# Kernel optimization log

Measured on AMD Instinct MI355X. Metric: run time of the kernel, lower is better.

Reference implementation:

```python
import jax, jax.numpy as jnp
import numpy as np

B, D_IN, H, D_OUT = 1024, 512, 512, 512


def _act(v):
    # torch.relu(x) ** 2
    r = jnp.maximum(v, 0.0)
    return r * r


def setup_inputs() -> dict:
    key = jax.random.key(0)
    ks = jax.random.split(key, 8)
    x = jax.random.normal(ks[0], (B, D_IN), dtype=jnp.float32)
    # input_to_hidden: Linear(D_IN, H)
    W_in = jax.random.normal(ks[1], (D_IN, H), dtype=jnp.float32) / np.sqrt(D_IN)
    b_in = jax.random.normal(ks[2], (H,), dtype=jnp.float32) * 0.01
    # hidden_to_hidden[i]: Linear(1, H-i-1). Pack into padded arrays [H-1, H]
    # where row i, column j is the weight feeding output index j (valid only j > i).
    W_hh = jax.random.normal(ks[3], (H - 1, H), dtype=jnp.float32) * 0.02
    b_hh = jax.random.normal(ks[4], (H - 1, H), dtype=jnp.float32) * 0.01
    # hidden_to_output: Linear(H, D_OUT)
    W_out = jax.random.normal(ks[5], (H, D_OUT), dtype=jnp.float32) / np.sqrt(H)
    b_out = jax.random.normal(ks[6], (D_OUT,), dtype=jnp.float32) * 0.01
    return {"x": x, "W_in": W_in, "b_in": b_in, "W_hh": W_hh, "b_hh": b_hh,
            "W_out": W_out, "b_out": b_out}


def reference(x, W_in, b_in, W_hh, b_hh, W_out, b_out):
    h0 = _act(x @ W_in + b_in)  # [B, H]
    hid = h0.shape[1]
    col = jnp.arange(hid)

    def step(h, inp):
        i, w, b = inp  # w, b: [H] padded rows
        src = jnp.take(h, i, axis=1)  # [B], uses UPDATED h (strict sequential dep)
        contrib = _act(src[:, None] * w[None, :] + b[None, :])  # [B, H]
        mask = (col > i).astype(h.dtype)  # only columns i+1.. get updated
        return h + contrib * mask[None, :], None

    xs = (jnp.arange(hid - 1), W_hh, b_hh)
    h, _ = jax.lax.scan(step, h0, xs)
    return h @ W_out + b_out  # [B, D_OUT]
```

## Files before the change

kernel.cpp:

```cpp
#include <hip/hip_runtime.h>

#define B_SZ 1024
#define DIN 512
#define HH 512
#define DOUT 512

typedef short bf16x8 __attribute__((ext_vector_type(8)));
typedef float f32x4 __attribute__((ext_vector_type(4)));

__device__ __forceinline__ unsigned short f2bf(float f) {
    unsigned int u = __float_as_uint(f);
    u += 0x7FFFu + ((u >> 16) & 1u);
    return (unsigned short)(u >> 16);
}
__device__ __forceinline__ float bf2f(unsigned short s) {
    return __uint_as_float(((unsigned int)s) << 16);
}

__device__ __forceinline__ uint4 cvt8(const float4& a0, const float4& a1, int term) {
    const float av[8] = {a0.x, a0.y, a0.z, a0.w, a1.x, a1.y, a1.z, a1.w};
    unsigned int p[4];
    #pragma unroll
    for (int q = 0; q < 4; ++q) {
        float f0 = av[2 * q], f1 = av[2 * q + 1];
        unsigned short h0 = f2bf(f0), h1 = f2bf(f1);
        if (term == 1) { h0 = f2bf(f0 - bf2f(h0)); h1 = f2bf(f1 - bf2f(h1)); }
        p[q] = (unsigned int)h0 | ((unsigned int)h1 << 16);
    }
    uint4 v; v.x = p[0]; v.y = p[1]; v.z = p[2]; v.w = p[3];
    return v;
}

__device__ __forceinline__ void convW_body(const float* __restrict__ W,
                                           uint4* __restrict__ dst, int t) {
    const int lane = t & 63;
    const int fb   = t >> 6;
    const int ks   = fb >> 5;
    const int nf   = fb & 31;
    const int col  = nf * 16 + (lane & 15);
    const int kb   = ks * 32 + ((lane >> 4) << 3);
    const int term = kb >> 9;
    const int c0   = kb & 511;
    unsigned short o[8];
    #pragma unroll
    for (int j = 0; j < 8; ++j) {
        const float f = W[(size_t)(c0 + j) * 512 + col];
        unsigned short hi = f2bf(f);
        o[j] = (term == 2) ? f2bf(f - bf2f(hi)) : hi;
    }
    uint4 v;
    v.x = (unsigned int)o[0] | ((unsigned int)o[1] << 16);
    v.y = (unsigned int)o[2] | ((unsigned int)o[3] << 16);
    v.z = (unsigned int)o[4] | ((unsigned int)o[5] << 16);
    v.w = (unsigned int)o[6] | ((unsigned int)o[7] << 16);
    dst[t] = v;
}

template <int C>
__device__ __forceinline__ void pack_bulk(const float* __restrict__ W_hh,
                                          const float* __restrict__ b_hh,
                                          float2* __restrict__ wbk, int e) {
    constexpr int NK = 7 - C;
    constexpr int CB = (C==0?0:C==1?7:C==2?13:C==3?18:C==4?22:C==5?25:27) * 4096;
    const int s   = e / (NK * 64);
    const int rem = e - s * (NK * 64);
    const int row = 64 * C + s;
    const int col = 64 * (C + 1) + rem;
    float2 o;
    o.x = W_hh[(size_t)row * 512 + col];
    o.y = b_hh[(size_t)row * 512 + col];
    wbk[CB + e] = o;
}

__global__ __launch_bounds__(256)
void prep_all(const float* __restrict__ W_hh, const float* __restrict__ b_hh,
              float2* __restrict__ wdg, float2* __restrict__ wbk,
              const float* __restrict__ W_in, uint4* __restrict__ Bin,
              const float* __restrict__ W_out, uint4* __restrict__ Bout) {
    const int b = blockIdx.x;
    const int tid = threadIdx.x;
    if (b < 128) {
        const int idx = b * 256 + tid;
        const int i = idx >> 6, l = idx & 63;
        float2 o;
        if (i < 511 && l > (i & 63)) {
            const int col = ((i >> 6) << 6) + l;
            o.x = W_hh[(size_t)i * 512 + col];
            o.y = b_hh[(size_t)i * 512 + col];
        } else { o.x = 0.0f; o.y = -1.0f; }
        wdg[idx] = o;
    } else if (b < 576) {
        const int rb = b - 128;
        if      (rb < 112) pack_bulk<0>(W_hh, b_hh, wbk, (rb      ) * 256 + tid);
        else if (rb < 208) pack_bulk<1>(W_hh, b_hh, wbk, (rb - 112) * 256 + tid);
        else if (rb < 288) pack_bulk<2>(W_hh, b_hh, wbk, (rb - 208) * 256 + tid);
        else if (rb < 352) pack_bulk<3>(W_hh, b_hh, wbk, (rb - 288) * 256 + tid);
        else if (rb < 400) pack_bulk<4>(W_hh, b_hh, wbk, (rb - 352) * 256 + tid);
        else if (rb < 432) pack_bulk<5>(W_hh, b_hh, wbk, (rb - 400) * 256 + tid);
        else               pack_bulk<6>(W_hh, b_hh, wbk, (rb - 432) * 256 + tid);
    } else if (b < 960) {
        convW_body(W_in, Bin, (b - 576) * 256 + tid);
    } else {
        convW_body(W_out, Bout, (b - 960) * 256 + tid);
    }
}

template <bool ACT>
__global__ __launch_bounds__(512, 2)
void mfma_gemm(const float* __restrict__ A,
               const uint4* __restrict__ Bg,
               const float* __restrict__ bias,
               float* __restrict__ C) {
    __shared__ uint4 lds[2][768];
    const int tid  = threadIdx.x;
    const int lane = tid & 63;
    const int w    = tid >> 6;
    const int mfw  = w & 3;
    const int nfw  = w >> 2;
    const int mf0  = blockIdx.x * 4;
    const int nf0  = blockIdx.y * 2;

    const int ks_s = tid >> 8;
    const int mf_s = (tid >> 6) & 3;
    const int arow = (mf0 + mf_s) * 16 + (lane & 15);
    const int koff = (lane >> 4) << 3;
    const int bks  = tid >> 7;
    const int bnf  = (tid >> 6) & 1;

    float4 Ra0, Ra1; uint4 R2;
    auto stage = [&](int s) {
        const int kp = (s * 2 + ks_s) * 32 + koff;
        const int c  = kp & 511;
        Ra0 = *(const float4*)&A[(size_t)arow * 512 + c];
        Ra1 = *(const float4*)&A[(size_t)arow * 512 + c + 4];
        if (tid < 256)
            R2 = Bg[(size_t)((s * 2 + bks) * 32 + nf0 + bnf) * 64 + lane];
    };
    auto write_tile = [&](int buf, int s) {
        const int kp = (s * 2 + ks_s) * 32 + koff;
        lds[buf][ks_s * 256 + mf_s * 64 + lane] = cvt8(Ra0, Ra1, kp >> 9);
        if (tid < 256)
            lds[buf][512 + bks * 128 + bnf * 64 + lane] = R2;
    };

    f32x4 acc = {0.f, 0.f, 0.f, 0.f};

    stage(0);
    write_tile(0, 0);
    stage(1);
    __syncthreads();

    for (int s = 0; s < 24; ++s) {
        const int cur = s & 1;
        if (s + 1 < 24) write_tile(cur ^ 1, s + 1);
        if (s + 2 < 24) stage(s + 2);
        __builtin_amdgcn_sched_barrier(0);

        bf16x8 aF0 = *(const bf16x8*)&lds[cur][        mfw * 64 + lane];
        bf16x8 aF1 = *(const bf16x8*)&lds[cur][256   + mfw * 64 + lane];
        bf16x8 bF0 = *(const bf16x8*)&lds[cur][512   + nfw * 64 + lane];
        bf16x8 bF1 = *(const bf16x8*)&lds[cur][512+128 + nfw * 64 + lane];
        acc = __builtin_amdgcn_mfma_f32_16x16x32_bf16(aF0, bF0, acc, 0, 0, 0);
        acc = __builtin_amdgcn_mfma_f32_16x16x32_bf16(aF1, bF1, acc, 0, 0, 0);
        __syncthreads();
    }

    const int colg  = (nf0 + nfw) * 16 + (lane & 15);
    const float bv  = bias[colg];
    const int rbase = (mf0 + mfw) * 16 + ((lane >> 4) << 2);
    #pragma unroll
    for (int r = 0; r < 4; ++r) {
        float v = acc[r] + bv;
        if (ACT) { v = fmaxf(v, 0.f); v = v * v; }
        C[(size_t)(rbase + r) * 512 + colg] = v;
    }
}

template <int C>
__device__ __forceinline__ void scan_chunk(const float2* __restrict__ wdg,
                                           const float2* __restrict__ wbk,
                                           float hr[8], int lane) {
    constexpr int NK = 7 - C;
    constexpr int DD = 16;
    constexpr int D  = (NK >= 6) ? 4 : (NK >= 3) ? 8 : 16;
    constexpr int CB = (C==0?0:C==1?7:C==2?13:C==3?18:C==4?22:C==5?25:C==6?27:28) * 4096;

    const float2* dptr = wdg + (64 * C) * 64 + lane;
    const float2* bptr = wbk + CB + lane;

    __syncthreads();

    float2 Wd[DD];
    #pragma unroll
    for (int q = 0; q < DD; ++q) Wd[q] = dptr[q * 64];

    float2 Wb[NK > 0 ? D : 1][NK > 0 ? NK : 1];
    if constexpr (NK > 0) {
        #pragma unroll
        for (int q = 0; q < D; ++q)
            #pragma unroll
            for (int k = 0; k < NK; ++k)
                Wb[q][k] = bptr[(q * NK + k) * 64];
    }
    __builtin_amdgcn_sched_barrier(0);

    for (int t = 0; t < 64 / DD; ++t) {
        #pragma unroll
        for (int q = 0; q < DD; ++q) {
            const int s = t * DD + q;
            if (!(C == 7 && s == 63)) {
                const float hi = __uint_as_float(
                    __builtin_amdgcn_readlane(__float_as_uint(hr[C]), s));
                const float tv = fmaf(hi, Wd[q].x, Wd[q].y);
                const float rv = fmaxf(tv, 0.f);
                hr[C] = fmaf(rv, rv, hr[C]);
            }
            if (t + 1 < 64 / DD) Wd[q] = dptr[(s + DD) * 64];
        }
        __builtin_amdgcn_s_barrier();
    }

    if constexpr (NK > 0) {
        constexpr int NT = 64 / D;
        for (int t = 0; t < NT; ++t) {
            #pragma unroll
            for (int q = 0; q < D; ++q) {
                const int i = t * D + q;
                const float hi = __uint_as_float(
                    __builtin_amdgcn_readlane(__float_as_uint(hr[C]), i));
                #pragma unroll
                for (int k = 0; k < NK; ++k) {
                    const float tv = fmaf(hi, Wb[q][k].x, Wb[q][k].y);
                    const float rv = fmaxf(tv, 0.f);
                    hr[C + 1 + k] = fmaf(rv, rv, hr[C + 1 + k]);
                }
                if (t + 1 < NT) {
                    const float2* p = bptr + (size_t)(i + D) * (NK * 64);
                    #pragma unroll
                    for (int k = 0; k < NK; ++k)
                        Wb[q][k] = p[k * 64];
                }
            }
            __builtin_amdgcn_s_barrier();
        }
    }
}

__global__ __launch_bounds__(256, 1)
void scan_kernel(const float2* __restrict__ wdg, const float2* __restrict__ wbk,
                 float* __restrict__ h) {
    const int lane = threadIdx.x & 63;
    const int wave = threadIdx.x >> 6;
    const int row  = blockIdx.x * 4 + wave;
    float* hrow = h + (size_t)row * HH;

    float hr[8];
    #pragma unroll
    for (int k = 0; k < 8; ++k) hr[k] = hrow[lane + 64 * k];

    scan_chunk<0>(wdg, wbk, hr, lane);
    scan_chunk<1>(wdg, wbk, hr, lane);
    scan_chunk<2>(wdg, wbk, hr, lane);
    scan_chunk<3>(wdg, wbk, hr, lane);
    scan_chunk<4>(wdg, wbk, hr, lane);
    scan_chunk<5>(wdg, wbk, hr, lane);
    scan_chunk<6>(wdg, wbk, hr, lane);
    scan_chunk<7>(wdg, wbk, hr, lane);

    #pragma unroll
    for (int k = 0; k < 8; ++k) hrow[lane + 64 * k] = hr[k];
}

extern "C" void kernel_launch(void* const* d_in, const int* in_sizes, int n_in,
                              void* d_out, int out_size, void* d_ws, size_t ws_size,
                              hipStream_t stream) {
    const float* x     = (const float*)d_in[0];
    const float* W_in  = (const float*)d_in[1];
    const float* b_in  = (const float*)d_in[2];
    const float* W_hh  = (const float*)d_in[3];
    const float* b_hh  = (const float*)d_in[4];
    const float* W_out = (const float*)d_in[5];
    const float* b_out = (const float*)d_in[6];
    float* out = (float*)d_out;

    char* ws = (char*)d_ws;
    float2* wdg  = (float2*)ws;
    float2* wbk  = (float2*)(ws + 0x040000u);
    float*  h    = (float*)(ws + 0x120000u);
    uint4*  Bin  = (uint4*)(ws + 0x320000u);
    uint4*  Bout = (uint4*)(ws + 0x4A0000u);

    prep_all<<<dim3(1344), dim3(256), 0, stream>>>(W_hh, b_hh, wdg, wbk,
                                                   W_in, Bin, W_out, Bout);

    mfma_gemm<true><<<dim3(16, 16), dim3(512), 0, stream>>>(x, Bin, b_in, h);

    scan_kernel<<<dim3(256), dim3(256), 0, stream>>>(wdg, wbk, h);

    mfma_gemm<false><<<dim3(16, 16), dim3(512), 0, stream>>>(h, Bout, b_out, out);
}
```

Baseline: 175.5 us.

## Stage off-diagonal scan weights through double-buffered LDS shared by block waves

```diff
diff --git a/kernel.cpp b/kernel.cpp
--- a/kernel.cpp
+++ b/kernel.cpp
@@ -179,30 +179,37 @@
 template <int C>
 __device__ __forceinline__ void scan_chunk(const float2* __restrict__ wdg,
                                            const float2* __restrict__ wbk,
-                                           float hr[8], int lane) {
+                                           float2 (* __restrict__ sm)[3584],
+                                           float hr[8], int lane, int tid) {
     constexpr int NK = 7 - C;
     constexpr int DD = 16;
-    constexpr int D  = (NK >= 6) ? 4 : (NK >= 3) ? 8 : 16;
     constexpr int CB = (C==0?0:C==1?7:C==2?13:C==3?18:C==4?22:C==5?25:C==6?27:28) * 4096;
-
-    const float2* dptr = wdg + (64 * C) * 64 + lane;
-    const float2* bptr = wbk + CB + lane;
-
-    __syncthreads();
+    constexpr int TS = (NK >= 4) ? 8 : (NK >= 2) ? 16 : 32;
+    constexpr int NT = 64 / TS;
+    constexpr int IB = (NK > 0) ? (TS * NK / 8) : 1;
+
+    const float2* dptr  = wdg + (64 * C) * 64 + lane;
+    const float4* gbase = (const float4*)(wbk + CB);
+
+    float4 Rst[IB];
+    auto stageR = [&](int t) {
+        const float4* g = gbase + (size_t)t * (TS * NK * 32);
+        #pragma unroll
+        for (int u = 0; u < IB; ++u) Rst[u] = g[u * 256 + tid];
+    };
+    auto writeR = [&](int buf) {
+        float4* l = (float4*)&sm[buf][0];
+        #pragma unroll
+        for (int u = 0; u < IB; ++u) l[u * 256 + tid] = Rst[u];
+    };
+
+    if constexpr (NK > 0) stageR(0);
 
     float2 Wd[DD];
     #pragma unroll
     for (int q = 0; q < DD; ++q) Wd[q] = dptr[q * 64];
 
-    float2 Wb[NK > 0 ? D : 1][NK > 0 ? NK : 1];
-    if constexpr (NK > 0) {
-        #pragma unroll
-        for (int q = 0; q < D; ++q)
-            #pragma unroll
-            for (int k = 0; k < NK; ++k)
-                Wb[q][k] = bptr[(q * NK + k) * 64];
-    }
-    __builtin_amdgcn_sched_barrier(0);
+    if constexpr (NK > 0) { writeR(0); stageR(1); }
 
     for (int t = 0; t < 64 / DD; ++t) {
         #pragma unroll
@@ -217,31 +224,32 @@
             }
             if (t + 1 < 64 / DD) Wd[q] = dptr[(s + DD) * 64];
         }
-        __builtin_amdgcn_s_barrier();
     }
 
     if constexpr (NK > 0) {
-        constexpr int NT = 64 / D;
+        __syncthreads();
         for (int t = 0; t < NT; ++t) {
-            #pragma unroll
-            for (int q = 0; q < D; ++q) {
-                const int i = t * D + q;
+            const int cur = t & 1;
+            if (t + 1 < NT) writeR(cur ^ 1);
+            if (t + 2 < NT) stageR(t + 2);
+            __builtin_amdgcn_sched_barrier(0);
+
+            #pragma unroll 4
+            for (int s = 0; s < TS; ++s) {
                 const float hi = __uint_as_float(
-                    __builtin_amdgcn_readlane(__float_as_uint(hr[C]), i));
+                    __builtin_amdgcn_readlane(__float_as_uint(hr[C]), t * TS + s));
+                float2 wv[NK];
+                #pragma unroll
+                for (int k = 0; k < NK; ++k)
+                    wv[k] = sm[cur][(s * NK + k) * 64 + lane];
                 #pragma unroll
                 for (int k = 0; k < NK; ++k) {
-                    const float tv = fmaf(hi, Wb[q][k].x, Wb[q][k].y);
+                    const float tv = fmaf(hi, wv[k].x, wv[k].y);
                     const float rv = fmaxf(tv, 0.f);
                     hr[C + 1 + k] = fmaf(rv, rv, hr[C + 1 + k]);
                 }
-                if (t + 1 < NT) {
-                    const float2* p = bptr + (size_t)(i + D) * (NK * 64);
-                    #pragma unroll
-                    for (int k = 0; k < NK; ++k)
-                        Wb[q][k] = p[k * 64];
-                }
             }
-            __builtin_amdgcn_s_barrier();
+            __syncthreads();
         }
     }
 }
@@ -249,8 +257,10 @@
 __global__ __launch_bounds__(256, 1)
 void scan_kernel(const float2* __restrict__ wdg, const float2* __restrict__ wbk,
                  float* __restrict__ h) {
-    const int lane = threadIdx.x & 63;
-    const int wave = threadIdx.x >> 6;
+    __shared__ float2 sm[2][3584];
+    const int tid  = threadIdx.x;
+    const int lane = tid & 63;
+    const int wave = tid >> 6;
     const int row  = blockIdx.x * 4 + wave;
     float* hrow = h + (size_t)row * HH;
 
@@ -258,14 +268,14 @@
     #pragma unroll
     for (int k = 0; k < 8; ++k) hr[k] = hrow[lane + 64 * k];
 
-    scan_chunk<0>(wdg, wbk, hr, lane);
-    scan_chunk<1>(wdg, wbk, hr, lane);
-    scan_chunk<2>(wdg, wbk, hr, lane);
-    scan_chunk<3>(wdg, wbk, hr, lane);
-    scan_chunk<4>(wdg, wbk, hr, lane);
-    scan_chunk<5>(wdg, wbk, hr, lane);
-    scan_chunk<6>(wdg, wbk, hr, lane);
-    scan_chunk<7>(wdg, wbk, hr, lane);
+    scan_chunk<0>(wdg, wbk, sm, hr, lane, tid);
+    scan_chunk<1>(wdg, wbk, sm, hr, lane, tid);
+    scan_chunk<2>(wdg, wbk, sm, hr, lane, tid);
+    scan_chunk<3>(wdg, wbk, sm, hr, lane, tid);
+    scan_chunk<4>(wdg, wbk, sm, hr, lane, tid);
+    scan_chunk<5>(wdg, wbk, sm, hr, lane, tid);
+    scan_chunk<6>(wdg, wbk, sm, hr, lane, tid);
+    scan_chunk<7>(wdg, wbk, sm, hr, lane, tid);
 
     #pragma unroll
     for (int k = 0; k < 8; ++k) hrow[lane + 64 * k] = hr[k];
```

Result: slower. 192.4 us (+9.7%).

## Fuse all stages into one cooperative kernel and stage scan weights via LDS

Applied to the files above, without the earlier changes.

```diff
diff --git a/kernel.cpp b/kernel.cpp
--- a/kernel.cpp
+++ b/kernel.cpp
@@ -1,4 +1,7 @@
 #include <hip/hip_runtime.h>
+#include <hip/hip_cooperative_groups.h>
+
+namespace cg = cooperative_groups;
 
 #define B_SZ 1024
 #define DIN 512
@@ -29,6 +32,12 @@
     }
     uint4 v; v.x = p[0]; v.y = p[1]; v.z = p[2]; v.w = p[3];
     return v;
+}
+
+__device__ __forceinline__ void gload_lds16(const void* g, void* l) {
+    __builtin_amdgcn_global_load_lds(
+        (__attribute__((address_space(1))) void*)g,
+        (__attribute__((address_space(3))) void*)l, 16, 0, 0);
 }
 
 __device__ __forceinline__ void convW_body(const float* __restrict__ W,
@@ -72,53 +81,55 @@
     wbk[CB + e] = o;
 }
 
-__global__ __launch_bounds__(256)
-void prep_all(const float* __restrict__ W_hh, const float* __restrict__ b_hh,
-              float2* __restrict__ wdg, float2* __restrict__ wbk,
-              const float* __restrict__ W_in, uint4* __restrict__ Bin,
-              const float* __restrict__ W_out, uint4* __restrict__ Bout) {
-    const int b = blockIdx.x;
-    const int tid = threadIdx.x;
-    if (b < 128) {
-        const int idx = b * 256 + tid;
-        const int i = idx >> 6, l = idx & 63;
-        float2 o;
-        if (i < 511 && l > (i & 63)) {
-            const int col = ((i >> 6) << 6) + l;
-            o.x = W_hh[(size_t)i * 512 + col];
-            o.y = b_hh[(size_t)i * 512 + col];
-        } else { o.x = 0.0f; o.y = -1.0f; }
-        wdg[idx] = o;
-    } else if (b < 576) {
-        const int rb = b - 128;
-        if      (rb < 112) pack_bulk<0>(W_hh, b_hh, wbk, (rb      ) * 256 + tid);
-        else if (rb < 208) pack_bulk<1>(W_hh, b_hh, wbk, (rb - 112) * 256 + tid);
-        else if (rb < 288) pack_bulk<2>(W_hh, b_hh, wbk, (rb - 208) * 256 + tid);
-        else if (rb < 352) pack_bulk<3>(W_hh, b_hh, wbk, (rb - 288) * 256 + tid);
-        else if (rb < 400) pack_bulk<4>(W_hh, b_hh, wbk, (rb - 352) * 256 + tid);
-        else if (rb < 432) pack_bulk<5>(W_hh, b_hh, wbk, (rb - 400) * 256 + tid);
-        else               pack_bulk<6>(W_hh, b_hh, wbk, (rb - 432) * 256 + tid);
-    } else if (b < 960) {
-        convW_body(W_in, Bin, (b - 576) * 256 + tid);
-    } else {
-        convW_body(W_out, Bout, (b - 960) * 256 + tid);
+__device__ __forceinline__ void prep_phase(const float* __restrict__ W_hh,
+                                           const float* __restrict__ b_hh,
+                                           float2* __restrict__ wdg,
+                                           float2* __restrict__ wbk,
+                                           const float* __restrict__ W_in,
+                                           uint4* __restrict__ Bin,
+                                           const float* __restrict__ W_out,
+                                           uint4* __restrict__ Bout,
+                                           int bid, int tid) {
+    for (int gt = bid * 512 + tid; gt < 344064; gt += 131072) {
+        if (gt < 32768) {
+            const int i = gt >> 6, l = gt & 63;
+            float2 o;
+            if (i < 511 && l > (i & 63)) {
+                const int col = ((i >> 6) << 6) + l;
+                o.x = W_hh[(size_t)i * 512 + col];
+                o.y = b_hh[(size_t)i * 512 + col];
+            } else { o.x = 0.0f; o.y = -1.0f; }
+            wdg[gt] = o;
+        } else if (gt < 147456) {
+            const int e = gt - 32768;
+            if      (e < 28672)  pack_bulk<0>(W_hh, b_hh, wbk, e);
+            else if (e < 53248)  pack_bulk<1>(W_hh, b_hh, wbk, e - 28672);
+            else if (e < 73728)  pack_bulk<2>(W_hh, b_hh, wbk, e - 53248);
+            else if (e < 90112)  pack_bulk<3>(W_hh, b_hh, wbk, e - 73728);
+            else if (e < 102400) pack_bulk<4>(W_hh, b_hh, wbk, e - 90112);
+            else if (e < 110592) pack_bulk<5>(W_hh, b_hh, wbk, e - 102400);
+            else                 pack_bulk<6>(W_hh, b_hh, wbk, e - 110592);
+        } else if (gt < 245760) {
+            convW_body(W_in, Bin, gt - 147456);
+        } else {
+            convW_body(W_out, Bout, gt - 245760);
+        }
     }
 }
 
 template <bool ACT>
-__global__ __launch_bounds__(512, 2)
-void mfma_gemm(const float* __restrict__ A,
-               const uint4* __restrict__ Bg,
-               const float* __restrict__ bias,
-               float* __restrict__ C) {
-    __shared__ uint4 lds[2][768];
-    const int tid  = threadIdx.x;
+__device__ __forceinline__ void gemm_body(const float* __restrict__ A,
+                                          const uint4* __restrict__ Bg,
+                                          const float* __restrict__ bias,
+                                          float* __restrict__ Cc,
+                                          uint4 (*lds)[768],
+                                          int bx, int by, int tid) {
     const int lane = tid & 63;
     const int w    = tid >> 6;
     const int mfw  = w & 3;
     const int nfw  = w >> 2;
-    const int mf0  = blockIdx.x * 4;
-    const int nf0  = blockIdx.y * 2;
+    const int mf0  = bx * 4;
+    const int nf0  = by * 2;
 
     const int ks_s = tid >> 8;
     const int mf_s = (tid >> 6) & 3;
@@ -156,9 +167,9 @@
         if (s + 2 < 24) stage(s + 2);
         __builtin_amdgcn_sched_barrier(0);
 
-        bf16x8 aF0 = *(const bf16x8*)&lds[cur][        mfw * 64 + lane];
-        bf16x8 aF1 = *(const bf16x8*)&lds[cur][256   + mfw * 64 + lane];
-        bf16x8 bF0 = *(const bf16x8*)&lds[cur][512   + nfw * 64 + lane];
+        bf16x8 aF0 = *(const bf16x8*)&lds[cur][          mfw * 64 + lane];
+        bf16x8 aF1 = *(const bf16x8*)&lds[cur][256     + mfw * 64 + lane];
+        bf16x8 bF0 = *(const bf16x8*)&lds[cur][512     + nfw * 64 + lane];
         bf16x8 bF1 = *(const bf16x8*)&lds[cur][512+128 + nfw * 64 + lane];
         acc = __builtin_amdgcn_mfma_f32_16x16x32_bf16(aF0, bF0, acc, 0, 0, 0);
         acc = __builtin_amdgcn_mfma_f32_16x16x32_bf16(aF1, bF1, acc, 0, 0, 0);
@@ -172,103 +183,141 @@
     for (int r = 0; r < 4; ++r) {
         float v = acc[r] + bv;
         if (ACT) { v = fmaxf(v, 0.f); v = v * v; }
-        C[(size_t)(rbase + r) * 512 + colg] = v;
+        Cc[(size_t)(rbase + r) * 512 + colg] = v;
     }
 }
 
 template <int C>
 __device__ __forceinline__ void scan_chunk(const float2* __restrict__ wdg,
                                            const float2* __restrict__ wbk,
-                                           float hr[8], int lane) {
+                                           float2* __restrict__ smb,
+                                           float hr[8], int lane, int wave, int tid) {
     constexpr int NK = 7 - C;
-    constexpr int DD = 16;
-    constexpr int D  = (NK >= 6) ? 4 : (NK >= 3) ? 8 : 16;
     constexpr int CB = (C==0?0:C==1?7:C==2?13:C==3?18:C==4?22:C==5?25:C==6?27:28) * 4096;
-
     const float2* dptr = wdg + (64 * C) * 64 + lane;
-    const float2* bptr = wbk + CB + lane;
-
-    __syncthreads();
-
-    float2 Wd[DD];
-    #pragma unroll
-    for (int q = 0; q < DD; ++q) Wd[q] = dptr[q * 64];
-
-    float2 Wb[NK > 0 ? D : 1][NK > 0 ? NK : 1];
+    const char* gchunk = (const char*)(wbk + CB);
+
+    float2 Wd[16];
+    if (wave < 4) {
+        #pragma unroll
+        for (int q = 0; q < 16; ++q) Wd[q] = dptr[q * 64];
+    }
     if constexpr (NK > 0) {
         #pragma unroll
-        for (int q = 0; q < D; ++q)
+        for (int u = 0; u < NK; ++u)
+            gload_lds16(gchunk + (size_t)(u * 512 + tid) * 16,
+                        (char*)smb + (size_t)(u * 512 + wave * 64) * 16);
+    }
+
+    if (wave < 4) {
+        for (int t = 0; t < 4; ++t) {
             #pragma unroll
-            for (int k = 0; k < NK; ++k)
-                Wb[q][k] = bptr[(q * NK + k) * 64];
-    }
-    __builtin_amdgcn_sched_barrier(0);
-
-    for (int t = 0; t < 64 / DD; ++t) {
-        #pragma unroll
-        for (int q = 0; q < DD; ++q) {
-            const int s = t * DD + q;
-            if (!(C == 7 && s == 63)) {
-                const float hi = __uint_as_float(
-                    __builtin_amdgcn_readlane(__float_as_uint(hr[C]), s));
-                const float tv = fmaf(hi, Wd[q].x, Wd[q].y);
-                const float rv = fmaxf(tv, 0.f);
-                hr[C] = fmaf(rv, rv, hr[C]);
+            for (int q = 0; q < 16; ++q) {
+                const int s = t * 16 + q;
+                if (!(C == 7 && s == 63)) {
+                    const float hi = __uint_as_float(
+                        __builtin_amdgcn_readlane(__float_as_uint(hr[C]), s));
+                    const float tv = fmaf(hi, Wd[q].x, Wd[q].y);
+                    const float rv = fmaxf(tv, 0.f);
+                    hr[C] = fmaf(rv, rv, hr[C]);
+                }
+                if (t < 3) Wd[q] = dptr[(s + 16) * 64];
             }
-            if (t + 1 < 64 / DD) Wd[q] = dptr[(s + DD) * 64];
         }
-        __builtin_amdgcn_s_barrier();
     }
 
     if constexpr (NK > 0) {
-        constexpr int NT = 64 / D;
-        for (int t = 0; t < NT; ++t) {
-            #pragma unroll
-            for (int q = 0; q < D; ++q) {
-                const int i = t * D + q;
-                const float hi = __uint_as_float(
-                    __builtin_amdgcn_readlane(__float_as_uint(hr[C]), i));
-                #pragma unroll
-                for (int k = 0; k < NK; ++k) {
-                    const float tv = fmaf(hi, Wb[q][k].x, Wb[q][k].y);
-                    const float rv = fmaxf(tv, 0.f);
-                    hr[C + 1 + k] = fmaf(rv, rv, hr[C + 1 + k]);
-                }
-                if (t + 1 < NT) {
-                    const float2* p = bptr + (size_t)(i + D) * (NK * 64);
+        __syncthreads();
+        for (int t = 0; t < 4; ++t) {
+            if (wave < 4) {
+                #pragma unroll 2
+                for (int s = 0; s < 16; ++s) {
+                    const float hi = __uint_as_float(
+                        __builtin_amdgcn_readlane(__float_as_uint(hr[C]), t * 16 + s));
                     #pragma unroll
-                    for (int k = 0; k < NK; ++k)
-                        Wb[q][k] = p[k * 64];
+                    for (int k = 0; k < NK; ++k) {
+                        const float2 wv = smb[(s * NK + k) * 64 + lane];
+                        const float tv = fmaf(hi, wv.x, wv.y);
+                        const float rv = fmaxf(tv, 0.f);
+                        hr[C + 1 + k] = fmaf(rv, rv, hr[C + 1 + k]);
+                    }
                 }
             }
-            __builtin_amdgcn_s_barrier();
+            __syncthreads();
+            if (t < 3) {
+                #pragma unroll
+                for (int u = 0; u < NK; ++u)
+                    gload_lds16(gchunk + (size_t)((t + 1) * NK * 512 + u * 512 + tid) * 16,
+                                (char*)smb + (size_t)(u * 512 + wave * 64) * 16);
+                __syncthreads();
+            }
         }
     }
 }
 
-__global__ __launch_bounds__(256, 1)
-void scan_kernel(const float2* __restrict__ wdg, const float2* __restrict__ wbk,
-                 float* __restrict__ h) {
-    const int lane = threadIdx.x & 63;
-    const int wave = threadIdx.x >> 6;
-    const int row  = blockIdx.x * 4 + wave;
-    float* hrow = h + (size_t)row * HH;
-
-    float hr[8];
-    #pragma unroll
-    for (int k = 0; k < 8; ++k) hr[k] = hrow[lane + 64 * k];
-
-    scan_chunk<0>(wdg, wbk, hr, lane);
-    scan_chunk<1>(wdg, wbk, hr, lane);
-    scan_chunk<2>(wdg, wbk, hr, lane);
-    scan_chunk<3>(wdg, wbk, hr, lane);
-    scan_chunk<4>(wdg, wbk, hr, lane);
-    scan_chunk<5>(wdg, wbk, hr, lane);
-    scan_chunk<6>(wdg, wbk, hr, lane);
-    scan_chunk<7>(wdg, wbk, hr, lane);
-
-    #pragma unroll
-    for (int k = 0; k < 8; ++k) hrow[lane + 64 * k] = hr[k];
+__device__ __forceinline__ void scan_phase(const float2* __restrict__ wdg,
+                                           const float2* __restrict__ wbk,
+                                           float* __restrict__ h,
+                                           float2* __restrict__ smb,
+                                           int bid, int tid) {
+    const int lane = tid & 63;
+    const int wave = tid >> 6;
+    float hr[8] = {0.f, 0.f, 0.f, 0.f, 0.f, 0.f, 0.f, 0.f};
+    float* hrow = h;
+    if (wave < 4) {
+        hrow = h + (size_t)(bid * 4 + wave) * HH;
+        #pragma unroll
+        for (int k = 0; k < 8; ++k) hr[k] = hrow[lane + 64 * k];
+    }
+    scan_chunk<0>(wdg, wbk, smb, hr, lane, wave, tid);
+    scan_chunk<1>(wdg, wbk, smb, hr, lane, wave, tid);
+    scan_chunk<2>(wdg, wbk, smb, hr, lane, wave, tid);
+    scan_chunk<3>(wdg, wbk, smb, hr, lane, wave, tid);
+    scan_chunk<4>(wdg, wbk, smb, hr, lane, wave, tid);
+    scan_chunk<5>(wdg, wbk, smb, hr, lane, wave, tid);
+    scan_chunk<6>(wdg, wbk, smb, hr, lane, wave, tid);
+    scan_chunk<7>(wdg, wbk, smb, hr, lane, wave, tid);
+    if (wave < 4) {
+        #pragma unroll
+        for (int k = 0; k < 8; ++k) hrow[lane + 64 * k] = hr[k];
+    }
+}
+
+__global__ __launch_bounds__(512, 2)
+void fused(const float* x, const float* W_in, const float* b_in,
+           const float* W_hh, const float* b_hh,
+           const float* W_out, const float* b_out,
+           float2* wdg, float2* wbk, float* h,
+           uint4* Bin, uint4* Bout, float* out) {
+    __shared__ __align__(16) float2 smem[7168];
+    const int tid = threadIdx.x;
+    const int bid = blockIdx.x;
+    cg::grid_group grid = cg::this_grid();
+
+    prep_phase(W_hh, b_hh, wdg, wbk, W_in, Bin, W_out, Bout, bid, tid);
+    grid.sync();
+    gemm_body<true>(x, Bin, b_in, h, (uint4(*)[768])smem, bid & 15, bid >> 4, tid);
+    grid.sync();
+    scan_phase(wdg, wbk, h, smem, bid, tid);
+    grid.sync();
+    gemm_body<false>(h, Bout, b_out, out, (uint4(*)[768])smem, bid & 15, bid >> 4, tid);
+}
+
+__global__ __launch_bounds__(512)
+void prep_k(const float* W_hh, const float* b_hh, float2* wdg, float2* wbk,
+            const float* W_in, uint4* Bin, const float* W_out, uint4* Bout) {
+    prep_phase(W_hh, b_hh, wdg, wbk, W_in, Bin, W_out, Bout, blockIdx.x, threadIdx.x);
+}
+template <bool ACT>
+__global__ __launch_bounds__(512, 2)
+void gemm_k(const float* A, const uint4* Bg, const float* bias, float* Cc) {
+    __shared__ uint4 lds[2][768];
+    gemm_body<ACT>(A, Bg, bias, Cc, lds, blockIdx.x & 15, blockIdx.x >> 4, threadIdx.x);
+}
+__global__ __launch_bounds__(512, 2)
+void scan_k(const float2* wdg, const float2* wbk, float* h) {
+    __shared__ __align__(16) float2 smem[7168];
+    scan_phase(wdg, wbk, h, smem, blockIdx.x, threadIdx.x);
 }
 
 extern "C" void kernel_launch(void* const* d_in, const int* in_sizes, int n_in,
@@ -290,12 +339,18 @@
     uint4*  Bin  = (uint4*)(ws + 0x320000u);
     uint4*  Bout = (uint4*)(ws + 0x4A0000u);
 
-    prep_all<<<dim3(1344), dim3(256), 0, stream>>>(W_hh, b_hh, wdg, wbk,
-                                                   W_in, Bin, W_out, Bout);
-
-    mfma_gemm<true><<<dim3(16, 16), dim3(512), 0, stream>>>(x, Bin, b_in, h);
-
-    scan_kernel<<<dim3(256), dim3(256), 0, stream>>>(wdg, wbk, h);
-
-    mfma_gemm<false><<<dim3(16, 16), dim3(512), 0, stream>>>(h, Bout, b_out, out);
-}
+    void* args[] = {(void*)&x, (void*)&W_in, (void*)&b_in, (void*)&W_hh,
+                    (void*)&b_hh, (void*)&W_out, (void*)&b_out,
+                    (void*)&wdg, (void*)&wbk, (void*)&h,
+                    (void*)&Bin, (void*)&Bout, (void*)&out};
+    hipError_t e = hipLaunchCooperativeKernel((const void*)fused, dim3(256),
+                                              dim3(512), args, 0, stream);
+    if (e != hipSuccess) {
+        (void)hipGetLastError();
+        prep_k<<<dim3(256), dim3(512), 0, stream>>>(W_hh, b_hh, wdg, wbk,
+                                                    W_in, Bin, W_out, Bout);
+        gemm_k<true><<<dim3(256), dim3(512), 0, stream>>>(x, Bin, b_in, h);
+        scan_k<<<dim3(256), dim3(512), 0, stream>>>(wdg, wbk, h);
+        gemm_k<false><<<dim3(256), dim3(512), 0, stream>>>(h, Bout, b_out, out);
+    }
+}
```

Measured after the change: 272.6 us. 1.55x slower.
